# Kernel tuning notes

Hardware: AMD Instinct MI355X
Metric: run time of the kernel (lower is better)

## Reference

```python
import jax, jax.numpy as jnp
import numpy as np

D_MODEL = 2048
N_HEADS = 16
HEAD_DIM = D_MODEL // N_HEADS


def setup_inputs() -> dict:
    key = jax.random.key(0)
    ks = jax.random.split(key, 5)
    scale = 1.0 / np.sqrt(D_MODEL)
    x = jax.random.normal(ks[0], (2, 2048, D_MODEL), dtype=jnp.float32)
    W_qkv = jax.random.normal(ks[1], (D_MODEL, 3 * D_MODEL), dtype=jnp.float32) * scale
    b_qkv = jnp.zeros((3 * D_MODEL,), dtype=jnp.float32)
    W_out = jax.random.normal(ks[2], (D_MODEL, D_MODEL), dtype=jnp.float32) * scale
    b_out = jnp.zeros((D_MODEL,), dtype=jnp.float32)
    return {"x": x, "W_qkv": W_qkv, "b_qkv": b_qkv, "W_out": W_out, "b_out": b_out}


def reference(x, W_qkv, b_qkv, W_out, b_out):
    bsz, seq_len, _ = x.shape
    # QKV projection: (b, s, 3*d) -> (3, b, h, s, hd)
    qkv = x @ W_qkv + b_qkv
    qkv = qkv.reshape(bsz, seq_len, 3, N_HEADS, HEAD_DIM)
    qkv = jnp.transpose(qkv, (2, 0, 3, 1, 4))
    q, k, v = qkv[0], qkv[1], qkv[2]
    # scaled dot-product scores: (b, h, s, s)
    scores = jnp.einsum("bhqd,bhkd->bhqk", q, k) / np.sqrt(HEAD_DIM).astype(np.float32)
    causal = jnp.tril(jnp.ones((seq_len, seq_len), dtype=bool))
    scores = jnp.where(causal[None, None], scores, -jnp.inf)
    attn = jax.nn.softmax(scores, axis=-1)
    # attention output: (b, h, s, hd) -> (b, s, d)
    out = jnp.einsum("bhqk,bhkd->bhqd", attn, v)
    out = jnp.transpose(out, (0, 2, 1, 3)).reshape(bsz, seq_len, D_MODEL)
    y = out @ W_out + b_out
    return y
```

## Files before the change

kernel.cpp:

```cpp
#include <hip/hip_runtime.h>
#include <stdint.h>
#include <stddef.h>


typedef __attribute__((ext_vector_type(8))) short bf16x8;
typedef __attribute__((ext_vector_type(4))) float f32x4;

#define SOFT_SCALE 0.12751743075419806f

__device__ __forceinline__ short f2bf(float f) {
  union { float f; unsigned u; } v; v.f = f;
  unsigned u = v.u + 0x7fffu + ((v.u >> 16) & 1u);
  return (short)(u >> 16);
}

__device__ __forceinline__ void gload_lds16(const void* g, const void* l) {
  __builtin_amdgcn_global_load_lds(
      (__attribute__((address_space(1))) void*)(uintptr_t)g,
      (__attribute__((address_space(3))) void*)(uintptr_t)l,
      16, 0, 0);
}

__global__ __launch_bounds__(256) void cast_f32_bf16(
    const float* __restrict__ in, short* __restrict__ out, int n8) {
  int i = blockIdx.x * 256 + threadIdx.x;
  if (i >= n8) return;
  float4 a = ((const float4*)in)[i * 2];
  float4 b = ((const float4*)in)[i * 2 + 1];
  bf16x8 o;
  o[0] = f2bf(a.x); o[1] = f2bf(a.y); o[2] = f2bf(a.z); o[3] = f2bf(a.w);
  o[4] = f2bf(b.x); o[5] = f2bf(b.y); o[6] = f2bf(b.z); o[7] = f2bf(b.w);
  ((bf16x8*)out)[i] = o;
}

__global__ __launch_bounds__(256) void transpose_cast_w(
    const float* __restrict__ W, short* __restrict__ WT, int K, int N) {
  __shared__ short t[32][33];
  int k0 = blockIdx.x * 32, n0 = blockIdx.y * 32;
  int r = threadIdx.x >> 3;
  int c = (threadIdx.x & 7) * 4;
  float4 v = *(const float4*)(W + (size_t)(k0 + r) * N + n0 + c);
  t[r][c + 0] = f2bf(v.x); t[r][c + 1] = f2bf(v.y);
  t[r][c + 2] = f2bf(v.z); t[r][c + 3] = f2bf(v.w);
  __syncthreads();
  short4 o;
  o.x = t[c + 0][r]; o.y = t[c + 1][r]; o.z = t[c + 2][r]; o.w = t[c + 3][r];
  *(short4*)(WT + (size_t)(n0 + r) * K + k0 + c) = o;
}

__global__ __launch_bounds__(512, 2) void gemm_qkv(
    const short* __restrict__ A, const short* __restrict__ BT,
    short* __restrict__ C, const float* __restrict__ bias,
    short* __restrict__ vTout, int M, int N, int K) {
  (void)M;
  __shared__ __align__(16) short SH[66048];
  const int tid = threadIdx.x;
  const int wave = tid >> 6, lane = tid & 63;
  const int quad = lane >> 4, l16 = lane & 15;
  const int wm = wave >> 2, wn = wave & 3;
  const int kx = (l16 & 7) << 3;

  const int gx = gridDim.x;
  int bid = blockIdx.y * gx + blockIdx.x;
  const int nwg = gx * gridDim.y;
  bid = (bid & 7) * (nwg >> 3) + (bid >> 3);
  const int m0 = (bid % gx) * 256, n0 = (bid / gx) * 256;

  const int rsub = lane >> 3;
  const int csub = ((lane & 7) ^ rsub) << 3;
  const int e1 = (wave & 3) + 8 * (wave >> 2);
  const int cA[4] = {wave, wave + 16, wave + 8, wave + 24};
  const int cB[4] = {e1, e1 + 16, e1 + 4, e1 + 20};
  const short* aP[4];
  const short* bP[4];
#pragma unroll
  for (int i = 0; i < 4; ++i) {
    aP[i] = A + (size_t)(m0 + cA[i] * 8 + rsub) * K + csub;
    bP[i] = BT + (size_t)(n0 + cB[i] * 8 + rsub) * K + csub;
  }

  auto stage = [&](int h, int st, int sbuf) {
    if (h == 0 || h == 2) {
      int i0 = (h == 0) ? 0 : 2;
#pragma unroll
      for (int i = 0; i < 2; ++i)
        gload_lds16(aP[i0 + i] + st * 64,
                    (const char*)SH + sbuf * 65536 + cA[i0 + i] * 1024);
    } else {
      int i0 = (h == 1) ? 0 : 2;
#pragma unroll
      for (int i = 0; i < 2; ++i)
        gload_lds16(bP[i0 + i] + st * 64,
                    (const char*)SH + sbuf * 65536 + 32768 + cB[i0 + i] * 1024);
    }
  };

  stage(0, 0, 0); stage(1, 0, 0); stage(2, 0, 0); stage(3, 0, 0);

  f32x4 acc[8][4] = {};
  const int nT = K >> 6;
  for (int t = 0; t < nT; ++t) {
    const int st = (t + 1 < nT) ? (t + 1) : (nT - 1);
    const int sbuf = (t + 1) & 1;
    const short* As = SH + (t & 1) * 32768;
    const short* Bs = As + 16384;
    bf16x8 bf[4][2];

    asm volatile("s_waitcnt vmcnt(4)" ::: "memory");
    __builtin_amdgcn_s_barrier();
    bf16x8 af0[4][2];
#pragma unroll
    for (int f = 0; f < 4; ++f) {
      const int row = wm * 128 + f * 16 + l16;
#pragma unroll
      for (int kk = 0; kk < 2; ++kk)
        af0[f][kk] = *(const bf16x8*)(As + row * 64 +
                                      (((kk << 5) | (quad << 3)) ^ kx));
    }
#pragma unroll
    for (int u = 0; u < 2; ++u) {
      const int row = wn * 64 + u * 16 + l16;
#pragma unroll
      for (int kk = 0; kk < 2; ++kk)
        bf[u][kk] = *(const bf16x8*)(Bs + row * 64 +
                                     (((kk << 5) | (quad << 3)) ^ kx));
    }
    stage(0, st, sbuf);
    __builtin_amdgcn_s_barrier();
    asm volatile("s_waitcnt lgkmcnt(0)" ::: "memory");
    __builtin_amdgcn_sched_barrier(0);
    __builtin_amdgcn_s_setprio(1);
#pragma unroll
    for (int f = 0; f < 4; ++f)
#pragma unroll
      for (int u = 0; u < 2; ++u)
#pragma unroll
        for (int kk = 0; kk < 2; ++kk)
          acc[f][u] = __builtin_amdgcn_mfma_f32_16x16x32_bf16(
              af0[f][kk], bf[u][kk], acc[f][u], 0, 0, 0);
    __builtin_amdgcn_s_setprio(0);

    asm volatile("s_waitcnt vmcnt(2)" ::: "memory");
    __builtin_amdgcn_s_barrier();
#pragma unroll
    for (int u = 0; u < 2; ++u) {
      const int row = wn * 64 + 32 + u * 16 + l16;
#pragma unroll
      for (int kk = 0; kk < 2; ++kk)
        bf[2 + u][kk] = *(const bf16x8*)(Bs + row * 64 +
                                         (((kk << 5) | (quad << 3)) ^ kx));
    }
    stage(1, st, sbuf);
    __builtin_amdgcn_s_barrier();
    asm volatile("s_waitcnt lgkmcnt(0)" ::: "memory");
    __builtin_amdgcn_sched_barrier(0);
    __builtin_amdgcn_s_setprio(1);
#pragma unroll
    for (int f = 0; f < 4; ++f)
#pragma unroll
      for (int u = 0; u < 2; ++u)
#pragma unroll
        for (int kk = 0; kk < 2; ++kk)
          acc[f][2 + u] = __builtin_amdgcn_mfma_f32_16x16x32_bf16(
              af0[f][kk], bf[2 + u][kk], acc[f][2 + u], 0, 0, 0);
    __builtin_amdgcn_s_setprio(0);

    __builtin_amdgcn_s_barrier();
    bf16x8 af1[4][2];
#pragma unroll
    for (int f = 0; f < 4; ++f) {
      const int row = wm * 128 + 64 + f * 16 + l16;
#pragma unroll
      for (int kk = 0; kk < 2; ++kk)
        af1[f][kk] = *(const bf16x8*)(As + row * 64 +
                                      (((kk << 5) | (quad << 3)) ^ kx));
    }
    stage(2, st, sbuf);
    __builtin_amdgcn_s_barrier();
    asm volatile("s_waitcnt lgkmcnt(0)" ::: "memory");
    __builtin_amdgcn_sched_barrier(0);
    __builtin_amdgcn_s_setprio(1);
#pragma unroll
    for (int f = 0; f < 4; ++f)
#pragma unroll
      for (int u = 0; u < 2; ++u)
#pragma unroll
        for (int kk = 0; kk < 2; ++kk)
          acc[4 + f][u] = __builtin_amdgcn_mfma_f32_16x16x32_bf16(
              af1[f][kk], bf[u][kk], acc[4 + f][u], 0, 0, 0);
    __builtin_amdgcn_s_setprio(0);

    __builtin_amdgcn_s_barrier();
    stage(3, st, sbuf);
    __builtin_amdgcn_s_setprio(1);
#pragma unroll
    for (int f = 0; f < 4; ++f)
#pragma unroll
      for (int u = 0; u < 2; ++u)
#pragma unroll
        for (int kk = 0; kk < 2; ++kk)
          acc[4 + f][2 + u] = __builtin_amdgcn_mfma_f32_16x16x32_bf16(
              af1[f][kk], bf[2 + u][kk], acc[4 + f][2 + u], 0, 0, 0);
    __builtin_amdgcn_s_setprio(0);
  }

  asm volatile("s_waitcnt vmcnt(0)" ::: "memory");
  __builtin_amdgcn_s_barrier();

  if (n0 >= 4096) {
    short* T = (short*)SH;
#pragma unroll
    for (int j = 0; j < 4; ++j) {
      const int nl = wn * 64 + j * 16 + l16;
      const float bv = bias[n0 + nl];
#pragma unroll
      for (int f = 0; f < 8; ++f) {
        const int ml = wm * 128 + f * 16 + quad * 4;
        short4 o;
        o.x = f2bf(acc[f][j][0] + bv);
        o.y = f2bf(acc[f][j][1] + bv);
        o.z = f2bf(acc[f][j][2] + bv);
        o.w = f2bf(acc[f][j][3] + bv);
        *(short4*)(T + nl * 258 + ml) = o;
      }
    }
    __builtin_amdgcn_s_barrier();
    const int b = m0 >> 11, s0 = m0 & 2047, h0 = (n0 - 4096) >> 7;
#pragma unroll
    for (int pass = 0; pass < 16; ++pass) {
      const int nl = pass * 16 + (tid >> 5);
      const int c = (tid & 31) * 8;
      bf16x8 v = *(const bf16x8*)(T + nl * 258 + c);
      *(bf16x8*)(vTout +
                 ((size_t)((b * 16 + h0 + (nl >> 7)) * 128 + (nl & 127))) *
                     2048 +
                 s0 + c) = v;
    }
    return;
  }

#pragma unroll
  for (int j = 0; j < 4; ++j) {
    const int n = n0 + wn * 64 + j * 16 + l16;
    const float bv = bias[n];
#pragma unroll
    for (int f = 0; f < 8; ++f) {
      const int mb = m0 + wm * 128 + f * 16 + quad * 4;
#pragma unroll
      for (int r = 0; r < 4; ++r) {
        float v = acc[f][j][r] + bv;
        if (n < 2048) v *= SOFT_SCALE;
        C[(size_t)(mb + r) * N + n] = f2bf(v);
      }
    }
  }
}

__global__ __launch_bounds__(512, 2) void gemm_out(
    const short* __restrict__ A, const short* __restrict__ BT,
    float* __restrict__ C, const float* __restrict__ bias, int M, int N,
    int K) {
  (void)M;
  __shared__ __align__(16) short SH[73728];
  const int tid = threadIdx.x;
  const int wave = tid >> 6, lane = tid & 63;
  const int quad = lane >> 4, l16 = lane & 15;
  const int wm = wave >> 1, wn = wave & 1;
  const int kx = (l16 & 7) << 3;

  const int gx = gridDim.x;
  int bid = blockIdx.y * gx + blockIdx.x;
  const int nwg = gx * gridDim.y;
  bid = (bid & 7) * (nwg >> 3) + (bid >> 3);
  const int m0 = (bid % gx) * 256, n0 = (bid / gx) * 128;

  const int rsub = lane >> 3;
  const int csub = ((lane & 7) ^ rsub) << 3;
  const short* aS[4];
  const short* bS[2];
#pragma unroll
  for (int i = 0; i < 4; ++i)
    aS[i] = A + (size_t)(m0 + (wave * 4 + i) * 8 + rsub) * K + csub;
#pragma unroll
  for (int i = 0; i < 2; ++i)
    bS[i] = BT + (size_t)(n0 + (wave * 2 + i) * 8 + rsub) * K + csub;

  auto stageA = [&](int st, int sb) {
#pragma unroll
    for (int i = 0; i < 4; ++i)
      gload_lds16(aS[i] + st * 64,
                  (const char*)SH + sb * 49152 + (wave * 4 + i) * 1024);
  };
  auto stageB = [&](int st, int sb) {
#pragma unroll
    for (int i = 0; i < 2; ++i)
      gload_lds16(bS[i] + st * 64,
                  (const char*)SH + sb * 49152 + 32768 + (wave * 2 + i) * 1024);
  };

  stageA(0, 0); stageB(0, 0);
  stageA(1, 1); stageB(1, 1);

  f32x4 acc[4][4] = {};
  const int nT = K >> 6;
  int buf = 0, sb = 2;
  for (int t = 0; t < nT; ++t) {
    const int st = (t + 2 < nT) ? (t + 2) : (nT - 1);
    const short* As = (const short*)((const char*)SH + buf * 49152);
    const short* Bs = As + 16384;

    asm volatile("s_waitcnt vmcnt(6)" ::: "memory");
    __builtin_amdgcn_s_barrier();

    bf16x8 af[4][2], bf[2][2];
#pragma unroll
    for (int f = 0; f < 4; ++f) {
      const int row = wm * 64 + f * 16 + l16;
#pragma unroll
      for (int kk = 0; kk < 2; ++kk)
        af[f][kk] = *(const bf16x8*)(As + row * 64 +
                                     (((kk << 5) | (quad << 3)) ^ kx));
    }
#pragma unroll
    for (int u = 0; u < 2; ++u) {
      const int row = wn * 64 + u * 16 + l16;
#pragma unroll
      for (int kk = 0; kk < 2; ++kk)
        bf[u][kk] = *(const bf16x8*)(Bs + row * 64 +
                                     (((kk << 5) | (quad << 3)) ^ kx));
    }
    stageA(st, sb);
    __builtin_amdgcn_s_barrier();
    asm volatile("s_waitcnt lgkmcnt(0)" ::: "memory");
    __builtin_amdgcn_sched_barrier(0);
    __builtin_amdgcn_s_setprio(1);
#pragma unroll
    for (int f = 0; f < 4; ++f)
#pragma unroll
      for (int u = 0; u < 2; ++u)
#pragma unroll
        for (int kk = 0; kk < 2; ++kk)
          acc[f][u] = __builtin_amdgcn_mfma_f32_16x16x32_bf16(
              af[f][kk], bf[u][kk], acc[f][u], 0, 0, 0);
    __builtin_amdgcn_s_setprio(0);
    __builtin_amdgcn_s_barrier();

#pragma unroll
    for (int u = 0; u < 2; ++u) {
      const int row = wn * 64 + 32 + u * 16 + l16;
#pragma unroll
      for (int kk = 0; kk < 2; ++kk)
        bf[u][kk] = *(const bf16x8*)(Bs + row * 64 +
                                     (((kk << 5) | (quad << 3)) ^ kx));
    }
    stageB(st, sb);
    __builtin_amdgcn_s_barrier();
    asm volatile("s_waitcnt lgkmcnt(0)" ::: "memory");
    __builtin_amdgcn_sched_barrier(0);
    __builtin_amdgcn_s_setprio(1);
#pragma unroll
    for (int f = 0; f < 4; ++f)
#pragma unroll
      for (int u = 0; u < 2; ++u)
#pragma unroll
        for (int kk = 0; kk < 2; ++kk)
          acc[f][2 + u] = __builtin_amdgcn_mfma_f32_16x16x32_bf16(
              af[f][kk], bf[u][kk], acc[f][2 + u], 0, 0, 0);
    __builtin_amdgcn_s_setprio(0);

    buf = (buf == 2) ? 0 : buf + 1;
    sb = (sb == 2) ? 0 : sb + 1;
  }

  asm volatile("s_waitcnt vmcnt(0)" ::: "memory");

#pragma unroll
  for (int j = 0; j < 4; ++j) {
    const int n = n0 + wn * 64 + j * 16 + l16;
    const float bv = bias[n];
#pragma unroll
    for (int f = 0; f < 4; ++f) {
      const int mb = m0 + wm * 64 + f * 16 + quad * 4;
#pragma unroll
      for (int r = 0; r < 4; ++r)
        C[(size_t)(mb + r) * N + n] = acc[f][j][r] + bv;
    }
  }
}

__global__ __launch_bounds__(512, 4) void attn_kernel(
    const short* __restrict__ qkv, const short* __restrict__ vT,
    short* __restrict__ obuf) {
  __shared__ __align__(16) short Ks[2 * 8192];
  __shared__ __align__(16) short Vs[2 * 8192];
  __shared__ __align__(16) short Ps[8192];
  const int tid = threadIdx.x;
  const int wave = tid >> 6, lane = tid & 63;
  const int quad = lane >> 4, l16 = lane & 15;
  const int bh = blockIdx.y, b = bh >> 4, h = bh & 15;
  const int px = blockIdx.x;
  const int p = (blockIdx.y & 16) ? (15 - px) : px;
  const int q0 = p * 128;
  const int nkt = 2 * (p + 1);

  const short* qbase = qkv + (size_t)b * 2048 * 6144 + h * 128;
  const short* kbase = qkv + (size_t)b * 2048 * 6144 + 2048 + h * 128;
  const short* vtbase = vT + (size_t)bh * 128 * 2048;
  short* obase = obuf + (size_t)b * 2048 * 2048 + h * 128;

  const int srow = lane >> 2;
  const int scol = (lane & 3) * 8;

  bf16x8 ones;
#pragma unroll
  for (int j = 0; j < 8; ++j) ones[j] = (short)0x3F80;

  bf16x8 qf[4];
#pragma unroll
  for (int kk = 0; kk < 4; ++kk)
    qf[kk] = *(const bf16x8*)(
        qbase + (size_t)(q0 + wave * 16 + l16) * 6144 + kk * 32 + quad * 8);

  f32x4 acco[8] = {};
  f32x4 accl = {};

  auto stage = [&](int buf, int kt) {
    const int k0 = kt * 64;
#pragma unroll
    for (int it = 0; it < 2; ++it) {
      int c = wave * 2 + it;
      gload_lds16(
          kbase + (size_t)(k0 + (c & 3) * 16 + srow) * 6144 + (c >> 2) * 32 +
              scol,
          (const char*)Ks + buf * 16384 + c * 1024);
    }
#pragma unroll
    for (int it = 0; it < 2; ++it) {
      int c = wave * 2 + it;
      gload_lds16(
          vtbase + (size_t)((c & 7) * 16 + srow) * 2048 + k0 + (c >> 3) * 32 +
              scol,
          (const char*)Vs + buf * 16384 + c * 1024);
    }
  };

  stage(0, 0);

  for (int kt = 0; kt < nkt; ++kt) {
    const int buf = kt & 1;
    __syncthreads();
    if (kt + 1 < nkt) stage(1 - buf, kt + 1);
    const short* KsB = Ks + buf * 8192;
    const short* VsB = Vs + buf * 8192;

    f32x4 accs[4] = {};
#pragma unroll
    for (int kk = 0; kk < 4; ++kk) {
      bf16x8 bfg[4];
#pragma unroll
      for (int tn = 0; tn < 4; ++tn)
        bfg[tn] = *(const bf16x8*)(KsB + (kk * 4 + tn) * 512 + l16 * 32 +
                                   quad * 8);
#pragma unroll
      for (int tn = 0; tn < 4; ++tn)
        accs[tn] = __builtin_amdgcn_mfma_f32_16x16x32_bf16(
            qf[kk], bfg[tn], accs[tn], 0, 0, 0);
    }

    if (kt >= nkt - 2) {
      const int k0 = kt * 64;
#pragma unroll
      for (int tn = 0; tn < 4; ++tn)
#pragma unroll
        for (int r = 0; r < 4; ++r) {
          int grow = q0 + wave * 16 + quad * 4 + r;
          int gcol = k0 + tn * 16 + l16;
          if (gcol > grow) accs[tn][r] = -1e30f;
        }
    }
#pragma unroll
    for (int tn = 0; tn < 4; ++tn)
#pragma unroll
      for (int r = 0; r < 4; ++r) accs[tn][r] = exp2f(accs[tn][r]);

#pragma unroll
    for (int r = 0; r < 4; ++r)
#pragma unroll
      for (int tn = 0; tn < 4; ++tn)
        Ps[wave * 1024 + (tn >> 1) * 512 + (quad * 4 + r) * 32 +
           (tn & 1) * 16 + l16] = f2bf(accs[tn][r]);

#pragma unroll
    for (int kk2 = 0; kk2 < 2; ++kk2) {
      bf16x8 av = *(const bf16x8*)(Ps + wave * 1024 + kk2 * 512 + l16 * 32 +
                                   quad * 8);
      accl = __builtin_amdgcn_mfma_f32_16x16x32_bf16(av, ones, accl, 0, 0, 0);
      bf16x8 bfg[8];
#pragma unroll
      for (int tn = 0; tn < 8; ++tn)
        bfg[tn] = *(const bf16x8*)(VsB + (kk2 * 8 + tn) * 512 + l16 * 32 +
                                   quad * 8);
#pragma unroll
      for (int tn = 0; tn < 8; ++tn)
        acco[tn] = __builtin_amdgcn_mfma_f32_16x16x32_bf16(
            av, bfg[tn], acco[tn], 0, 0, 0);
    }
  }

  float inv[4];
#pragma unroll
  for (int r = 0; r < 4; ++r) inv[r] = 1.f / accl[r];
#pragma unroll
  for (int r = 0; r < 4; ++r) {
    int row = q0 + wave * 16 + quad * 4 + r;
#pragma unroll
    for (int tn = 0; tn < 8; ++tn)
      obase[(size_t)row * 2048 + tn * 16 + l16] = f2bf(acco[tn][r] * inv[r]);
  }
}

extern "C" void kernel_launch(void* const* d_in, const int* in_sizes, int n_in,
                              void* d_out, int out_size, void* d_ws,
                              size_t ws_size, hipStream_t stream) {
  (void)in_sizes; (void)n_in; (void)out_size; (void)ws_size;
  const float* x    = (const float*)d_in[0];
  const float* Wqkv = (const float*)d_in[1];
  const float* bqkv = (const float*)d_in[2];
  const float* Wout = (const float*)d_in[3];
  const float* bout = (const float*)d_in[4];
  float* out = (float*)d_out;

  char* ws = (char*)d_ws;
  short* xb    = (short*)(ws);
  short* wqkvT = (short*)(ws + 16777216);
  short* woutT = (short*)(ws + 41943040);
  short* qkv   = (short*)(ws + 50331648);
  short* vTb   = (short*)(ws + 100663296);
  short* obuf  = (short*)(ws + 117440512);

  cast_f32_bf16<<<4096, 256, 0, stream>>>(x, xb, 1048576);
  transpose_cast_w<<<dim3(64, 192), 256, 0, stream>>>(Wqkv, wqkvT, 2048, 6144);
  transpose_cast_w<<<dim3(64, 64), 256, 0, stream>>>(Wout, woutT, 2048, 2048);

  gemm_qkv<<<dim3(16, 24), 512, 0, stream>>>(
      xb, wqkvT, qkv, bqkv, vTb, 4096, 6144, 2048);

  attn_kernel<<<dim3(16, 32), 512, 0, stream>>>(qkv, vTb, obuf);

  gemm_out<<<dim3(16, 16), 512, 0, stream>>>(
      obuf, woutT, out, bout, 4096, 2048, 2048);
}
```

Baseline: 373.0 us.

## Widen QKV GEMM tile to 256x384 to cut grid to one wave

The QKV projection GEMM tile grows from 256x256 to 256x384, so the grid shrinks from 384 to 256 workgroups, matching the CU count in a single wave, and each workgroup reuses its A tile across more columns. LDS staging, the B-load mapping, accumulators (8x6 fragments per wave) and the wait counts are all reworked for the wider tile. The epilogue now handles tiles that straddle the K/V boundary by writing Q/K columns directly and transposing V heads through LDS one 128-column head at a time. It raises register and LDS pressure, which may limit occupancy to one workgroup per CU, and the per-head epilogue adds barriers.

```diff
diff --git a/kernel.cpp b/kernel.cpp
--- a/kernel.cpp
+++ b/kernel.cpp
@@ -53,7 +53,7 @@
     short* __restrict__ C, const float* __restrict__ bias,
     short* __restrict__ vTout, int M, int N, int K) {
   (void)M;
-  __shared__ __align__(16) short SH[66048];
+  __shared__ __align__(16) short SH[81920];
   const int tid = threadIdx.x;
   const int wave = tid >> 6, lane = tid & 63;
   const int quad = lane >> 4, l16 = lane & 15;
@@ -64,49 +64,54 @@
   int bid = blockIdx.y * gx + blockIdx.x;
   const int nwg = gx * gridDim.y;
   bid = (bid & 7) * (nwg >> 3) + (bid >> 3);
-  const int m0 = (bid % gx) * 256, n0 = (bid / gx) * 256;
+  const int m0 = (bid % gx) * 256, n0 = (bid / gx) * 384;
 
   const int rsub = lane >> 3;
   const int csub = ((lane & 7) ^ rsub) << 3;
-  const int e1 = (wave & 3) + 8 * (wave >> 2);
   const int cA[4] = {wave, wave + 16, wave + 8, wave + 24};
-  const int cB[4] = {e1, e1 + 16, e1 + 4, e1 + 20};
+  int cB[6];
+#pragma unroll
+  for (int j = 0; j < 3; ++j) {
+    int i = wave * 3 + j;
+    cB[j] = 12 * (i / 6) + (i % 6);
+    cB[3 + j] = cB[j] + 6;
+  }
   const short* aP[4];
-  const short* bP[4];
-#pragma unroll
-  for (int i = 0; i < 4; ++i) {
+  const short* bP[6];
+#pragma unroll
+  for (int i = 0; i < 4; ++i)
     aP[i] = A + (size_t)(m0 + cA[i] * 8 + rsub) * K + csub;
-    bP[i] = BT + (size_t)(n0 + cB[i] * 8 + rsub) * K + csub;
-  }
-
-  auto stage = [&](int h, int st, int sbuf) {
-    if (h == 0 || h == 2) {
-      int i0 = (h == 0) ? 0 : 2;
+#pragma unroll
+  for (int j = 0; j < 6; ++j)
+    bP[j] = BT + (size_t)(n0 + cB[j] * 8 + rsub) * K + csub;
+
+  auto stage = [&](int g, int st, int sbuf) {
+    char* base = (char*)SH + sbuf * 81920;
+    if (g == 0 || g == 2) {
+      int i0 = (g == 0) ? 0 : 2;
 #pragma unroll
       for (int i = 0; i < 2; ++i)
-        gload_lds16(aP[i0 + i] + st * 64,
-                    (const char*)SH + sbuf * 65536 + cA[i0 + i] * 1024);
+        gload_lds16(aP[i0 + i] + st * 64, base + cA[i0 + i] * 1024);
     } else {
-      int i0 = (h == 1) ? 0 : 2;
-#pragma unroll
-      for (int i = 0; i < 2; ++i)
-        gload_lds16(bP[i0 + i] + st * 64,
-                    (const char*)SH + sbuf * 65536 + 32768 + cB[i0 + i] * 1024);
+      int j0 = (g == 1) ? 0 : 3;
+#pragma unroll
+      for (int j = 0; j < 3; ++j)
+        gload_lds16(bP[j0 + j] + st * 64, base + 32768 + cB[j0 + j] * 1024);
     }
   };
 
   stage(0, 0, 0); stage(1, 0, 0); stage(2, 0, 0); stage(3, 0, 0);
 
-  f32x4 acc[8][4] = {};
+  f32x4 acc[8][6] = {};
   const int nT = K >> 6;
   for (int t = 0; t < nT; ++t) {
     const int st = (t + 1 < nT) ? (t + 1) : (nT - 1);
     const int sbuf = (t + 1) & 1;
-    const short* As = SH + (t & 1) * 32768;
+    const short* As = SH + (t & 1) * 40960;
     const short* Bs = As + 16384;
-    bf16x8 bf[4][2];
-
-    asm volatile("s_waitcnt vmcnt(4)" ::: "memory");
+    bf16x8 bf[6][2];
+
+    asm volatile("s_waitcnt vmcnt(5)" ::: "memory");
     __builtin_amdgcn_s_barrier();
     bf16x8 af0[4][2];
 #pragma unroll
@@ -118,8 +123,8 @@
                                       (((kk << 5) | (quad << 3)) ^ kx));
     }
 #pragma unroll
-    for (int u = 0; u < 2; ++u) {
-      const int row = wn * 64 + u * 16 + l16;
+    for (int u = 0; u < 3; ++u) {
+      const int row = wn * 96 + u * 16 + l16;
 #pragma unroll
       for (int kk = 0; kk < 2; ++kk)
         bf[u][kk] = *(const bf16x8*)(Bs + row * 64 +
@@ -133,7 +138,7 @@
 #pragma unroll
     for (int f = 0; f < 4; ++f)
 #pragma unroll
-      for (int u = 0; u < 2; ++u)
+      for (int u = 0; u < 3; ++u)
 #pragma unroll
         for (int kk = 0; kk < 2; ++kk)
           acc[f][u] = __builtin_amdgcn_mfma_f32_16x16x32_bf16(
@@ -143,11 +148,11 @@
     asm volatile("s_waitcnt vmcnt(2)" ::: "memory");
     __builtin_amdgcn_s_barrier();
 #pragma unroll
-    for (int u = 0; u < 2; ++u) {
-      const int row = wn * 64 + 32 + u * 16 + l16;
-#pragma unroll
-      for (int kk = 0; kk < 2; ++kk)
-        bf[2 + u][kk] = *(const bf16x8*)(Bs + row * 64 +
+    for (int u = 0; u < 3; ++u) {
+      const int row = wn * 96 + 48 + u * 16 + l16;
+#pragma unroll
+      for (int kk = 0; kk < 2; ++kk)
+        bf[3 + u][kk] = *(const bf16x8*)(Bs + row * 64 +
                                          (((kk << 5) | (quad << 3)) ^ kx));
     }
     stage(1, st, sbuf);
@@ -158,11 +163,11 @@
 #pragma unroll
     for (int f = 0; f < 4; ++f)
 #pragma unroll
-      for (int u = 0; u < 2; ++u)
+      for (int u = 0; u < 3; ++u)
 #pragma unroll
         for (int kk = 0; kk < 2; ++kk)
-          acc[f][2 + u] = __builtin_amdgcn_mfma_f32_16x16x32_bf16(
-              af0[f][kk], bf[2 + u][kk], acc[f][2 + u], 0, 0, 0);
+          acc[f][3 + u] = __builtin_amdgcn_mfma_f32_16x16x32_bf16(
+              af0[f][kk], bf[3 + u][kk], acc[f][3 + u], 0, 0, 0);
     __builtin_amdgcn_s_setprio(0);
 
     __builtin_amdgcn_s_barrier();
@@ -183,7 +188,7 @@
 #pragma unroll
     for (int f = 0; f < 4; ++f)
 #pragma unroll
-      for (int u = 0; u < 2; ++u)
+      for (int u = 0; u < 3; ++u)
 #pragma unroll
         for (int kk = 0; kk < 2; ++kk)
           acc[4 + f][u] = __builtin_amdgcn_mfma_f32_16x16x32_bf16(
@@ -196,62 +201,73 @@
 #pragma unroll
     for (int f = 0; f < 4; ++f)
 #pragma unroll
-      for (int u = 0; u < 2; ++u)
+      for (int u = 0; u < 3; ++u)
 #pragma unroll
         for (int kk = 0; kk < 2; ++kk)
-          acc[4 + f][2 + u] = __builtin_amdgcn_mfma_f32_16x16x32_bf16(
-              af1[f][kk], bf[2 + u][kk], acc[4 + f][2 + u], 0, 0, 0);
+          acc[4 + f][3 + u] = __builtin_amdgcn_mfma_f32_16x16x32_bf16(
+              af1[f][kk], bf[3 + u][kk], acc[4 + f][3 + u], 0, 0, 0);
     __builtin_amdgcn_s_setprio(0);
   }
 
   asm volatile("s_waitcnt vmcnt(0)" ::: "memory");
   __builtin_amdgcn_s_barrier();
 
-  if (n0 >= 4096) {
+  if (n0 < 4096) {
+#pragma unroll
+    for (int j = 0; j < 6; ++j) {
+      const int n = n0 + wn * 96 + j * 16 + l16;
+      if (n < 4096) {
+        const float bv = bias[n];
+#pragma unroll
+        for (int f = 0; f < 8; ++f) {
+          const int mb = m0 + wm * 128 + f * 16 + quad * 4;
+#pragma unroll
+          for (int r = 0; r < 4; ++r) {
+            float v = acc[f][j][r] + bv;
+            if (n < 2048) v *= SOFT_SCALE;
+            C[(size_t)(mb + r) * N + n] = f2bf(v);
+          }
+        }
+      }
+    }
+  }
+
+  if (n0 + 384 > 4096) {
     short* T = (short*)SH;
-#pragma unroll
-    for (int j = 0; j < 4; ++j) {
-      const int nl = wn * 64 + j * 16 + l16;
-      const float bv = bias[n0 + nl];
-#pragma unroll
-      for (int f = 0; f < 8; ++f) {
-        const int ml = wm * 128 + f * 16 + quad * 4;
-        short4 o;
-        o.x = f2bf(acc[f][j][0] + bv);
-        o.y = f2bf(acc[f][j][1] + bv);
-        o.z = f2bf(acc[f][j][2] + bv);
-        o.w = f2bf(acc[f][j][3] + bv);
-        *(short4*)(T + nl * 258 + ml) = o;
+    const int b = m0 >> 11, s0 = m0 & 2047;
+#pragma unroll
+    for (int hh = 0; hh < 3; ++hh) {
+      const int nlb = hh * 128;
+      const int gcol = n0 + nlb;
+      if (gcol < 4096) continue;
+      const int hg = (gcol - 4096) >> 7;
+#pragma unroll
+      for (int j = 0; j < 6; ++j) {
+        const int nl = wn * 96 + j * 16 + l16;
+        if (nl >= nlb && nl < nlb + 128) {
+          const float bv = bias[n0 + nl];
+#pragma unroll
+          for (int f = 0; f < 8; ++f) {
+            const int ml = wm * 128 + f * 16 + quad * 4;
+            short4 o;
+            o.x = f2bf(acc[f][j][0] + bv);
+            o.y = f2bf(acc[f][j][1] + bv);
+            o.z = f2bf(acc[f][j][2] + bv);
+            o.w = f2bf(acc[f][j][3] + bv);
+            *(short4*)(T + (nl - nlb) * 264 + ml) = o;
+          }
+        }
       }
-    }
-    __builtin_amdgcn_s_barrier();
-    const int b = m0 >> 11, s0 = m0 & 2047, h0 = (n0 - 4096) >> 7;
-#pragma unroll
-    for (int pass = 0; pass < 16; ++pass) {
-      const int nl = pass * 16 + (tid >> 5);
-      const int c = (tid & 31) * 8;
-      bf16x8 v = *(const bf16x8*)(T + nl * 258 + c);
-      *(bf16x8*)(vTout +
-                 ((size_t)((b * 16 + h0 + (nl >> 7)) * 128 + (nl & 127))) *
-                     2048 +
-                 s0 + c) = v;
-    }
-    return;
-  }
-
-#pragma unroll
-  for (int j = 0; j < 4; ++j) {
-    const int n = n0 + wn * 64 + j * 16 + l16;
-    const float bv = bias[n];
-#pragma unroll
-    for (int f = 0; f < 8; ++f) {
-      const int mb = m0 + wm * 128 + f * 16 + quad * 4;
-#pragma unroll
-      for (int r = 0; r < 4; ++r) {
-        float v = acc[f][j][r] + bv;
-        if (n < 2048) v *= SOFT_SCALE;
-        C[(size_t)(mb + r) * N + n] = f2bf(v);
+      __builtin_amdgcn_s_barrier();
+#pragma unroll
+      for (int pass = 0; pass < 8; ++pass) {
+        const int row = pass * 16 + (tid >> 5);
+        const int c = (tid & 31) * 8;
+        bf16x8 v = *(const bf16x8*)(T + row * 264 + c);
+        *(bf16x8*)(vTout + ((size_t)((b * 16 + hg) * 128 + row)) * 2048 + s0 +
+                   c) = v;
       }
+      __builtin_amdgcn_s_barrier();
     }
   }
 }
@@ -542,7 +558,7 @@
   transpose_cast_w<<<dim3(64, 192), 256, 0, stream>>>(Wqkv, wqkvT, 2048, 6144);
   transpose_cast_w<<<dim3(64, 64), 256, 0, stream>>>(Wout, woutT, 2048, 2048);
 
-  gemm_qkv<<<dim3(16, 24), 512, 0, stream>>>(
+  gemm_qkv<<<dim3(16, 16), 512, 0, stream>>>(
       xb, wqkvT, qkv, bqkv, vTb, 4096, 6144, 2048);
 
   attn_kernel<<<dim3(16, 32), 512, 0, stream>>>(qkv, vTb, obuf);
```

Result: slower. 606.0 us (+62.5%).
